# Optimization experiments

Hardware: AMD Instinct MI355X
Metric: run time of the kernel (lower is better)

Reference implementation:

```python
import jax, jax.numpy as jnp
import numpy as np

D_MODEL = 1024
D_STATE = 16
D_CONV = 4
EXPAND = 2
D_INNER = D_MODEL * EXPAND          # 2048
DT_RANK = max(1, D_MODEL // 16)     # 64
BATCH, SEQ = 4, 2048


def setup_inputs() -> dict:
    key = jax.random.key(0)
    ks = jax.random.split(key, 8)
    s = lambda n: 1.0 / np.sqrt(n)
    x = jax.random.normal(ks[0], (BATCH, SEQ, D_MODEL), jnp.float32)
    in_proj_w = jax.random.normal(ks[1], (2 * D_INNER, D_MODEL), jnp.float32) * s(D_MODEL)
    conv_w = jax.random.normal(ks[2], (D_INNER, 1, D_CONV), jnp.float32) * s(D_CONV)
    conv_b = jax.random.normal(ks[3], (D_INNER,), jnp.float32) * 0.01
    x_proj_w = jax.random.normal(ks[4], (DT_RANK + 2 * D_STATE, D_INNER), jnp.float32) * s(D_INNER)
    dt_proj_w = jax.random.normal(ks[5], (D_INNER, DT_RANK), jnp.float32) * s(DT_RANK)
    dt_proj_b = jax.random.normal(ks[6], (D_INNER,), jnp.float32) * 0.01
    A_log = jnp.broadcast_to(jnp.log(jnp.arange(1, D_STATE + 1, dtype=jnp.float32))[None, :],
                             (D_INNER, D_STATE)).copy()
    D_param = jnp.ones((D_INNER,), jnp.float32)
    out_proj_w = jax.random.normal(ks[7], (D_MODEL, D_INNER), jnp.float32) * s(D_INNER)
    return {"x": x, "in_proj_w": in_proj_w, "conv_w": conv_w, "conv_b": conv_b,
            "x_proj_w": x_proj_w, "dt_proj_w": dt_proj_w, "dt_proj_b": dt_proj_b,
            "A_log": A_log, "D_param": D_param, "out_proj_w": out_proj_w}


def _ssm_forward(x, in_proj_w, conv_w, conv_b, x_proj_w, dt_proj_w, dt_proj_b,
                 A_log, D_param, out_proj_w):
    B, L, _ = x.shape
    # input projection -> (B, L, 2*D_INNER), split into x_ssm and gate z
    xz = jnp.einsum('bld,ed->ble', x, in_proj_w)
    x_ssm, z = xz[..., :D_INNER], xz[..., D_INNER:]
    # causal depthwise conv1d (torch pads both sides then slices [:L] == left pad only)
    xc = jnp.transpose(x_ssm, (0, 2, 1))  # (B, D_INNER, L)
    xc = jax.lax.conv_general_dilated(
        xc, conv_w, window_strides=(1,), padding=[(D_CONV - 1, 0)],
        dimension_numbers=('NCH', 'OIH', 'NCH'), feature_group_count=D_INNER)
    xc = xc + conv_b[None, :, None]
    x_ssm = jax.nn.silu(jnp.transpose(xc, (0, 2, 1)))  # (B, L, D_INNER)
    # input-dependent dt, B, C
    dbl = jnp.einsum('bld,ed->ble', x_ssm, x_proj_w)  # (B, L, DT_RANK+2N)
    dt_x = dbl[..., :DT_RANK]
    B_x = dbl[..., DT_RANK:DT_RANK + D_STATE]
    C_x = dbl[..., DT_RANK + D_STATE:]
    dt = jax.nn.softplus(jnp.einsum('blr,dr->bld', dt_x, dt_proj_w) + dt_proj_b)  # (B, L, D_INNER)
    A = -jnp.exp(A_log)  # (D_INNER, D_STATE)

    # selective scan over L with lax.scan; carry h: (B, D_INNER, D_STATE)
    def step(h, inp):
        dt_t, B_t, C_t, x_t = inp  # (B,D), (B,N), (B,N), (B,D)
        dA = jnp.exp(dt_t[:, :, None] * A[None, :, :])          # (B, D, N)
        dB = dt_t[:, :, None] * B_t[:, None, :]                 # (B, D, N)
        h = dA * h + dB * x_t[:, :, None]
        y_t = jnp.einsum('bdn,bn->bd', h, C_t)
        return h, y_t

    h0 = jnp.zeros((B, D_INNER, D_STATE), x.dtype)
    xs = (jnp.moveaxis(dt, 1, 0), jnp.moveaxis(B_x, 1, 0),
          jnp.moveaxis(C_x, 1, 0), jnp.moveaxis(x_ssm, 1, 0))
    _, ys = jax.lax.scan(step, h0, xs)          # ys: (L, B, D_INNER)
    y = jnp.moveaxis(ys, 0, 1) + D_param[None, None, :] * x_ssm
    y = y * jax.nn.silu(z)
    return jnp.einsum('ble,de->bld', y, out_proj_w)


def reference(x, in_proj_w, conv_w, conv_b, x_proj_w, dt_proj_w, dt_proj_b,
              A_log, D_param, out_proj_w):
    return _ssm_forward(x, in_proj_w, conv_w, conv_b, x_proj_w, dt_proj_w,
                        dt_proj_b, A_log, D_param, out_proj_w)
```

## Files before the change

kernel.cpp:

```cpp
#include <hip/hip_runtime.h>
#include <hip/hip_bf16.h>
#include <math.h>

#define D_MODEL 1024
#define D_STATE 16
#define D_CONV 4
#define D_INNER 2048
#define DT_RANK 64
#define BATCH 4
#define SEQ 2048
#define ML (BATCH * SEQ)
#define NCH 64
#define CL (SEQ / NCH)

typedef __attribute__((ext_vector_type(8))) short short8;
typedef __attribute__((ext_vector_type(8))) unsigned short u16x8;
typedef __attribute__((ext_vector_type(4))) float f32x4;

__device__ __forceinline__ float bf2f(unsigned short u) {
  union { unsigned int i; float f; } v;
  v.i = ((unsigned int)u) << 16;
  return v.f;
}
__device__ __forceinline__ unsigned short f2bf(float f) {
  union { float f; unsigned int i; } u;
  u.f = f;
  unsigned int r = u.i + 0x7fffu + ((u.i >> 16) & 1u);
  return (unsigned short)(r >> 16);
}
__device__ __forceinline__ unsigned int f2bf_pk(float a, float b) {
  union { __hip_bfloat162 h; unsigned int u; } cv;
  cv.h = __float22bfloat162_rn(make_float2(a, b));
  return cv.u;
}
template <bool BF>
__device__ __forceinline__ float ld1(const void* p, size_t i) {
  if constexpr (BF) return bf2f(((const unsigned short*)p)[i]);
  else return ((const float*)p)[i];
}
template <bool BF>
__device__ __forceinline__ void ld4(const void* p, size_t i, float o[4]) {
  if constexpr (BF) {
    ushort4 v = *(const ushort4*)((const unsigned short*)p + i);
    o[0] = bf2f(v.x); o[1] = bf2f(v.y); o[2] = bf2f(v.z); o[3] = bf2f(v.w);
  } else {
    float4 v = *(const float4*)((const float*)p + i);
    o[0] = v.x; o[1] = v.y; o[2] = v.z; o[3] = v.w;
  }
}

__device__ __forceinline__ void gl_lds16(const unsigned short* g,
                                         unsigned short* l) {
  __builtin_amdgcn_global_load_lds(
      (const __attribute__((address_space(1))) void*)g,
      (__attribute__((address_space(3))) void*)l, 16, 0, 0);
}

#define CVT_N0 (ML * 1024)
#define CVT_N1 (4096 * 1024)
#define CVT_N2 (1024 * 2048)
#define CVT_N3 (2048 * 64)
#define CVT_N4 (128 * 2048)
#define CVT_E0 CVT_N0
#define CVT_E1 (CVT_E0 + CVT_N1)
#define CVT_E2 (CVT_E1 + CVT_N2)
#define CVT_E3 (CVT_E2 + CVT_N3)
#define CVT_E4 (CVT_E3 + CVT_N4)

__device__ __forceinline__ void cvt4(const void* in, size_t i,
                                     unsigned short* out, size_t o, int bf) {
  if (bf) {
    *(ushort4*)(out + o) = *(const ushort4*)((const unsigned short*)in + i);
  } else {
    float4 f = *(const float4*)((const float*)in + i);
    uint2 v;
    v.x = f2bf_pk(f.x, f.y);
    v.y = f2bf_pk(f.z, f.w);
    *(uint2*)(out + o) = v;
  }
}

__global__ __launch_bounds__(256) void cvt_all_kernel(
    const void* __restrict__ x, const void* __restrict__ ipw,
    const void* __restrict__ opw, const void* __restrict__ dtw,
    const void* __restrict__ xpw, unsigned short* __restrict__ x_bf,
    unsigned short* __restrict__ ipw_bf, unsigned short* __restrict__ opw_bf,
    unsigned short* __restrict__ dtw_bf, unsigned short* __restrict__ xpw_pad,
    int* __restrict__ flag) {
  __shared__ int cnt;
  if (threadIdx.x == 0) cnt = 0;
  __syncthreads();
  {
    const unsigned int wv = ((const unsigned int*)x)[threadIdx.x];
    const unsigned int e = (wv >> 7) & 0xffu;
    if (e < 100u || e > 145u) atomicAdd(&cnt, 1);
  }
  __syncthreads();
  const int bf = (cnt < 32) ? 1 : 0;
  if (blockIdx.x == 0 && threadIdx.x == 0) flag[0] = bf;

  const size_t g = (size_t)(blockIdx.x * 256 + threadIdx.x) * 4;
  if (g < CVT_E0) {
    cvt4(x, g, x_bf, g, bf);
  } else if (g < CVT_E1) {
    const size_t i = g - CVT_E0;
    cvt4(ipw, i, ipw_bf, i, bf);
  } else if (g < CVT_E2) {
    const size_t i = g - CVT_E1;
    cvt4(opw, i, opw_bf, i, bf);
  } else if (g < CVT_E3) {
    const size_t i = g - CVT_E2;
    cvt4(dtw, i, dtw_bf, i, bf);
  } else if (g < CVT_E4) {
    const size_t i = g - CVT_E3;
    const int row = (int)(i >> 11);
    if (row < 96) {
      cvt4(xpw, i, xpw_pad, i, bf);
    } else {
      ushort4 z = {0, 0, 0, 0};
      *(ushort4*)(xpw_pad + i) = z;
    }
  }
}

#define K1_LDA 1024
#define K1_NT 16

#define K1_STG(srcbase, lds, t_, h_)                                       \
  {                                                                        \
    const unsigned short* s_ =                                             \
        (srcbase) + (size_t)(h_) * (128 * K1_LDA) + (size_t)(t_) * 64;     \
    unsigned short* d_ = (lds) + (((t_) & 1) * 2 + (h_)) * 8192 + w * 512; \
    gl_lds16(s_, d_);                                                      \
    gl_lds16(s_ + 64 * K1_LDA, d_ + 4096);                                 \
  }

__global__ __launch_bounds__(512, 2) void gemm256_k1(
    const unsigned short* __restrict__ A,
    const unsigned short* __restrict__ B,
    unsigned short* __restrict__ C) {
  __shared__ unsigned short As[32768];
  __shared__ unsigned short Bs[32768];
  const int tid = threadIdx.x;
  const int l = tid & 63, w = tid >> 6;
  const int bid = blockIdx.x;
  const int swz = (bid & 7) * 64 + (bid >> 3);
  const int m0 = (swz >> 4) * 256, n0 = (swz & 15) * 256;
  const int row0 = tid >> 3;
  const int c0 = (tid & 7) ^ (row0 & 7);
  const unsigned short* aSrc = A + (size_t)(m0 + row0) * K1_LDA + c0 * 8;
  const unsigned short* bSrc = B + (size_t)(n0 + row0) * K1_LDA + c0 * 8;
  const int q = l >> 4, mr = l & 15;
  const int wm = w >> 2, wn = w & 3;

  K1_STG(aSrc, As, 0, 0);
  K1_STG(aSrc, As, 0, 1);
  K1_STG(bSrc, Bs, 0, 0);
  K1_STG(bSrc, Bs, 0, 1);
  K1_STG(bSrc, Bs, 1, 0);
  K1_STG(bSrc, Bs, 1, 1);
  K1_STG(aSrc, As, 1, 0);
  asm volatile("s_waitcnt vmcnt(6)" ::: "memory");
  asm volatile("s_barrier" ::: "memory");

  f32x4 acc[8][4] = {};
  for (int t = 0; t < K1_NT; ++t) {
    const int tb = (t & 1) * 2;
    short8 bfr[4][2];
#pragma unroll
    for (int ni = 0; ni < 4; ++ni)
#pragma unroll
      for (int kk = 0; kk < 2; ++kk) {
        const int r = (wn & 1) * 64 + ni * 16 + mr;
        const int c = kk * 4 + q;
        bfr[ni][kk] = *(const short8*)&Bs[(tb + (wn >> 1)) * 8192 + r * 64 +
                                          ((c ^ (r & 7)) * 8)];
      }
#pragma unroll
    for (int p = 0; p < 4; ++p) {
      short8 af[2][2];
#pragma unroll
      for (int i = 0; i < 2; ++i)
#pragma unroll
        for (int kk = 0; kk < 2; ++kk) {
          const int r = (2 * p + i) * 16 + mr;
          const int c = kk * 4 + q;
          af[i][kk] = *(const short8*)&As[(tb + wm) * 8192 + r * 64 +
                                          ((c ^ (r & 7)) * 8)];
        }
      if (p == 0) {
        if (t + 1 < K1_NT) K1_STG(aSrc, As, t + 1, 1);
      } else if (p == 1) {
        if (t + 2 < K1_NT) K1_STG(bSrc, Bs, t + 2, 0);
      } else if (p == 2) {
        if (t + 2 < K1_NT) K1_STG(bSrc, Bs, t + 2, 1);
      } else {
        if (t + 2 < K1_NT) K1_STG(aSrc, As, t + 2, 0);
      }
      asm volatile("s_barrier" ::: "memory");
      __builtin_amdgcn_s_setprio(1);
#pragma unroll
      for (int i = 0; i < 2; ++i)
#pragma unroll
        for (int ni = 0; ni < 4; ++ni)
#pragma unroll
          for (int kk = 0; kk < 2; ++kk)
            acc[2 * p + i][ni] = __builtin_amdgcn_mfma_f32_16x16x32_bf16(
                af[i][kk], bfr[ni][kk], acc[2 * p + i][ni], 0, 0, 0);
      __builtin_amdgcn_s_setprio(0);
      if (p == 3) {
        if (t + 2 < K1_NT) {
          asm volatile("s_waitcnt vmcnt(6)" ::: "memory");
        } else {
          asm volatile("s_waitcnt vmcnt(0)" ::: "memory");
        }
      }
      asm volatile("s_barrier" ::: "memory");
    }
  }
#pragma unroll
  for (int mi = 0; mi < 8; ++mi) {
#pragma unroll
    for (int ni = 0; ni < 4; ++ni) {
      const int row = m0 + wm * 128 + mi * 16 + q * 4;
      const int col = n0 + wn * 64 + ni * 16 + mr;
      const size_t off0 = (size_t)row * 4096 + col;
      const unsigned int p01 = f2bf_pk(acc[mi][ni][0], acc[mi][ni][1]);
      const unsigned int p23 = f2bf_pk(acc[mi][ni][2], acc[mi][ni][3]);
      C[off0] = (unsigned short)p01;
      C[off0 + 4096] = (unsigned short)(p01 >> 16);
      C[off0 + 2 * 4096] = (unsigned short)p23;
      C[off0 + 3 * 4096] = (unsigned short)(p23 >> 16);
    }
  }
}

#define K6_LDA 2048
#define K6_NT 32

#define K6_STGA(t_, h_)                                                 \
  {                                                                     \
    const unsigned short* s_ =                                          \
        aSrc + (size_t)(h_) * (128 * K6_LDA) + (size_t)(t_) * 64;       \
    unsigned short* d_ = As + (((t_) & 1) * 2 + (h_)) * 8192 + w * 512; \
    gl_lds16(s_, d_);                                                   \
    gl_lds16(s_ + 64 * K6_LDA, d_ + 4096);                              \
  }
#define K6_STGB(t_)                                            \
  {                                                            \
    const unsigned short* s_ = bSrc + (size_t)(t_) * 64;       \
    unsigned short* d_ = Bs6 + ((t_) & 1) * 8192 + w * 512;    \
    gl_lds16(s_, d_);                                          \
    gl_lds16(s_ + 64 * K6_LDA, d_ + 4096);                     \
  }

__global__ __launch_bounds__(512, 2) void gemm256x128_k6(
    const unsigned short* __restrict__ A,
    const unsigned short* __restrict__ B,
    void* __restrict__ C,
    const int* __restrict__ flag) {
  __shared__ unsigned short As[32768];
  __shared__ unsigned short Bs6[16384];
  const int tid = threadIdx.x;
  const int l = tid & 63, w = tid >> 6;
  const int bid = blockIdx.x;
  const int swz = (bid & 7) * 32 + (bid >> 3);
  const int n0 = (swz & 7) * 128, m0 = (swz >> 3) * 256;
  const int row0 = tid >> 3;
  const int c0 = (tid & 7) ^ (row0 & 7);
  const unsigned short* aSrc = A + (size_t)(m0 + row0) * K6_LDA + c0 * 8;
  const unsigned short* bSrc = B + (size_t)(n0 + row0) * K6_LDA + c0 * 8;
  const int q = l >> 4, mr = l & 15;
  const int wm = w >> 2, wn = w & 3;

  K6_STGA(0, 0);
  K6_STGA(0, 1);
  K6_STGB(0);
  K6_STGB(1);
  K6_STGA(1, 0);
  asm volatile("s_waitcnt vmcnt(4)" ::: "memory");
  asm volatile("s_barrier" ::: "memory");

  f32x4 acc[8][2] = {};
  for (int t = 0; t < K6_NT; ++t) {
    const int tb = (t & 1) * 2;
    short8 bfr[2][2];
#pragma unroll
    for (int ni = 0; ni < 2; ++ni)
#pragma unroll
      for (int kk = 0; kk < 2; ++kk) {
        const int r = wn * 32 + ni * 16 + mr;
        const int c = kk * 4 + q;
        bfr[ni][kk] = *(const short8*)&Bs6[(t & 1) * 8192 + r * 64 +
                                           ((c ^ (r & 7)) * 8)];
      }
#pragma unroll
    for (int p = 0; p < 4; ++p) {
      short8 af[2][2];
#pragma unroll
      for (int i = 0; i < 2; ++i)
#pragma unroll
        for (int kk = 0; kk < 2; ++kk) {
          const int r = (2 * p + i) * 16 + mr;
          const int c = kk * 4 + q;
          af[i][kk] = *(const short8*)&As[(tb + wm) * 8192 + r * 64 +
                                          ((c ^ (r & 7)) * 8)];
        }
      if (p == 0) {
        if (t + 1 < K6_NT) K6_STGA(t + 1, 1);
      } else if (p == 1) {
        if (t + 2 < K6_NT) K6_STGB(t + 2);
      } else if (p == 3) {
        if (t + 2 < K6_NT) K6_STGA(t + 2, 0);
      }
      asm volatile("s_barrier" ::: "memory");
      __builtin_amdgcn_s_setprio(1);
#pragma unroll
      for (int i = 0; i < 2; ++i)
#pragma unroll
        for (int ni = 0; ni < 2; ++ni)
#pragma unroll
          for (int kk = 0; kk < 2; ++kk)
            acc[2 * p + i][ni] = __builtin_amdgcn_mfma_f32_16x16x32_bf16(
                af[i][kk], bfr[ni][kk], acc[2 * p + i][ni], 0, 0, 0);
      __builtin_amdgcn_s_setprio(0);
      if (p == 3) {
        if (t + 2 < K6_NT) {
          asm volatile("s_waitcnt vmcnt(4)" ::: "memory");
        } else {
          asm volatile("s_waitcnt vmcnt(0)" ::: "memory");
        }
      }
      asm volatile("s_barrier" ::: "memory");
    }
  }
  const int bf = *flag;
#pragma unroll
  for (int mi = 0; mi < 8; ++mi) {
#pragma unroll
    for (int ni = 0; ni < 2; ++ni) {
      const int row = m0 + wm * 128 + mi * 16 + q * 4;
      const int col = n0 + wn * 32 + ni * 16 + mr;
      const size_t off0 = (size_t)row * 1024 + col;
      if (bf) {
        const unsigned int p01 = f2bf_pk(acc[mi][ni][0], acc[mi][ni][1]);
        const unsigned int p23 = f2bf_pk(acc[mi][ni][2], acc[mi][ni][3]);
        unsigned short* C16 = (unsigned short*)C;
        C16[off0] = (unsigned short)p01;
        C16[off0 + 1024] = (unsigned short)(p01 >> 16);
        C16[off0 + 2 * 1024] = (unsigned short)p23;
        C16[off0 + 3 * 1024] = (unsigned short)(p23 >> 16);
      } else {
        float* Cf = (float*)C;
#pragma unroll
        for (int j = 0; j < 4; ++j)
          Cf[off0 + (size_t)j * 1024] = acc[mi][ni][j];
      }
    }
  }
}

__global__ __launch_bounds__(256) void dt_gemm_kernel(
    const unsigned short* __restrict__ Adbl,
    const unsigned short* __restrict__ Bw,
    unsigned short* __restrict__ Cdt,
    const void* __restrict__ bias, const int* __restrict__ flag) {
  __shared__ unsigned short Bs[128 * 64];
  __shared__ unsigned short Ass[4][128 * 64];
  const int tid = threadIdx.x;
  const int l = tid & 63, w = tid >> 6;
  const int bn = blockIdx.x * 128;
  const int mg = blockIdx.y * 512;
  const int srow = tid >> 3;
  const int sc = ((tid & 7) ^ (srow & 7)) * 8;
  const unsigned short* aSrc = Adbl + (size_t)(mg + srow) * 128 + sc;
  const unsigned short* bSrc = Bw + (size_t)(bn + srow) * 64 + sc;
#define K4_STGB(i_) gl_lds16(bSrc + (i_) * 32 * 64, Bs + (i_)*2048 + w * 512)
#define K4_STGA(mt_, i_)                                  \
  gl_lds16(aSrc + (size_t)((mt_)*128 + (i_)*32) * 128,    \
           Ass[(mt_) & 3] + (i_)*2048 + w * 512)
  K4_STGB(0); K4_STGB(1); K4_STGB(2); K4_STGB(3);
  K4_STGA(0, 0); K4_STGA(0, 1); K4_STGA(0, 2); K4_STGA(0, 3);
  K4_STGA(1, 0); K4_STGA(1, 1); K4_STGA(1, 2); K4_STGA(1, 3);
  asm volatile("s_waitcnt vmcnt(4)" ::: "memory");
  asm volatile("s_barrier" ::: "memory");
  const int q = l >> 4, mr = l & 15;
  const int wm = w >> 1, wn = w & 1;
  short8 bfr[4][2];
#pragma unroll
  for (int ni = 0; ni < 4; ++ni)
#pragma unroll
    for (int kk = 0; kk < 2; ++kk) {
      const int r = wn * 64 + ni * 16 + mr;
      const int c = kk * 4 + q;
      bfr[ni][kk] = *(const short8*)&Bs[r * 64 + ((c ^ (r & 7)) * 8)];
    }
  const int bf = *flag;
  float bv[4];
#pragma unroll
  for (int ni = 0; ni < 4; ++ni) {
    const int col = bn + wn * 64 + ni * 16 + mr;
    bv[ni] = bf ? ld1<true>(bias, col) : ld1<false>(bias, col);
  }
#pragma unroll
  for (int mt = 0; mt < 4; ++mt) {
    if (mt + 2 < 4) {
      K4_STGA(mt + 2, 0); K4_STGA(mt + 2, 1);
      K4_STGA(mt + 2, 2); K4_STGA(mt + 2, 3);
    }
    short8 af[4][2];
#pragma unroll
    for (int mi = 0; mi < 4; ++mi)
#pragma unroll
      for (int kk = 0; kk < 2; ++kk) {
        const int r = wm * 64 + mi * 16 + mr;
        const int c = kk * 4 + q;
        af[mi][kk] =
            *(const short8*)&Ass[mt & 3][r * 64 + ((c ^ (r & 7)) * 8)];
      }
    f32x4 acc[4][4] = {};
#pragma unroll
    for (int mi = 0; mi < 4; ++mi)
#pragma unroll
      for (int ni = 0; ni < 4; ++ni)
#pragma unroll
        for (int kk = 0; kk < 2; ++kk)
          acc[mi][ni] = __builtin_amdgcn_mfma_f32_16x16x32_bf16(
              af[mi][kk], bfr[ni][kk], acc[mi][ni], 0, 0, 0);
#pragma unroll
    for (int mi = 0; mi < 4; ++mi) {
#pragma unroll
      for (int ni = 0; ni < 4; ++ni) {
        const int row = mg + mt * 128 + wm * 64 + mi * 16 + q * 4;
        const int col = bn + wn * 64 + ni * 16 + mr;
        const size_t off0 = (size_t)row * 4096 + col;
        float v[4];
#pragma unroll
        for (int j = 0; j < 4; ++j) {
          const float t = acc[mi][ni][j] + bv[ni];
          v[j] = fmaxf(t, 0.f) + __logf(1.f + __expf(-fabsf(t)));
        }
        const unsigned int p01 = f2bf_pk(v[0], v[1]);
        const unsigned int p23 = f2bf_pk(v[2], v[3]);
        Cdt[off0] = (unsigned short)p01;
        Cdt[off0 + 4096] = (unsigned short)(p01 >> 16);
        Cdt[off0 + 2 * 4096] = (unsigned short)p23;
        Cdt[off0 + 3 * 4096] = (unsigned short)(p23 >> 16);
      }
    }
    if (mt + 2 < 4) {
      asm volatile("s_waitcnt vmcnt(4)" ::: "memory");
    } else {
      asm volatile("s_waitcnt vmcnt(0)" ::: "memory");
    }
    if (mt < 3) asm volatile("s_barrier" ::: "memory");
  }
}

template <int EPI, int TAG>
__global__ __launch_bounds__(256) void gemm_mfma(
    const unsigned short* __restrict__ Ain, int lda,
    const unsigned short* __restrict__ Bin, int ldb, void* __restrict__ C,
    int ldc, int K, const void* __restrict__ bias,
    const int* __restrict__ flag) {
  __shared__ unsigned short As[128 * 32];
  __shared__ unsigned short Bs[128 * 32];
  const unsigned short* A = Ain;
  const unsigned short* B = Bin;
  if (EPI == 3) {
    A += (size_t)blockIdx.z * 512;
    B += (size_t)blockIdx.z * 512;
  }
  const int tid = threadIdx.x;
  const int l = tid & 63, w = tid >> 6;
  const int bm = blockIdx.y * 128;
  const int bn = blockIdx.x * 128;
  const int r0 = w * 16 + (l >> 2);
  const int cc = (((l & 3) ^ ((l >> 2) & 3) ^ ((l >> 4) & 3))) * 8;
  const unsigned short* Ap0 = A + (size_t)(bm + r0) * lda + cc;
  const unsigned short* Ap1 = A + (size_t)(bm + r0 + 64) * lda + cc;
  const unsigned short* Bp0 = B + (size_t)(bn + r0) * ldb + cc;
  const unsigned short* Bp1 = B + (size_t)(bn + r0 + 64) * ldb + cc;
  const int q = l >> 4, mr = l & 15;
  const int wm = w >> 1, wn = w & 1;
  const int slot = (q ^ (mr & 3) ^ (mr >> 2)) * 8;
  f32x4 acc[4][4] = {};
  for (int k0 = 0; k0 < K; k0 += 32) {
    gl_lds16(Ap0 + k0, As + w * 512);
    gl_lds16(Ap1 + k0, As + 2048 + w * 512);
    gl_lds16(Bp0 + k0, Bs + w * 512);
    gl_lds16(Bp1 + k0, Bs + 2048 + w * 512);
    __syncthreads();
    short8 af[4], bfr[4];
#pragma unroll
    for (int mi = 0; mi < 4; ++mi)
      af[mi] = *(const short8*)&As[(wm * 64 + mi * 16 + mr) * 32 + slot];
#pragma unroll
    for (int ni = 0; ni < 4; ++ni)
      bfr[ni] = *(const short8*)&Bs[(wn * 64 + ni * 16 + mr) * 32 + slot];
#pragma unroll
    for (int mi = 0; mi < 4; ++mi)
#pragma unroll
      for (int ni = 0; ni < 4; ++ni)
        acc[mi][ni] = __builtin_amdgcn_mfma_f32_16x16x32_bf16(
            af[mi], bfr[ni], acc[mi][ni], 0, 0, 0);
    __syncthreads();
  }
  const int bf = (EPI == 1) ? *flag : 0;
  float* Cp3 = (EPI == 3)
                   ? ((float*)C + (size_t)blockIdx.z * ML * 128)
                   : (float*)C;
#pragma unroll
  for (int mi = 0; mi < 4; ++mi) {
#pragma unroll
    for (int ni = 0; ni < 4; ++ni) {
      const int row = bm + wm * 64 + mi * 16 + q * 4;
      const int col = bn + wn * 64 + ni * 16 + mr;
      const size_t off0 = (size_t)row * ldc + col;
      if (EPI == 0) {
        const unsigned int p01 = f2bf_pk(acc[mi][ni][0], acc[mi][ni][1]);
        const unsigned int p23 = f2bf_pk(acc[mi][ni][2], acc[mi][ni][3]);
        unsigned short* C16 = (unsigned short*)C;
        C16[off0] = (unsigned short)p01;
        C16[off0 + ldc] = (unsigned short)(p01 >> 16);
        C16[off0 + 2 * (size_t)ldc] = (unsigned short)p23;
        C16[off0 + 3 * (size_t)ldc] = (unsigned short)(p23 >> 16);
      } else if (EPI == 3) {
#pragma unroll
        for (int j = 0; j < 4; ++j)
          Cp3[off0 + (size_t)j * ldc] = acc[mi][ni][j];
      } else {
        if (bf) {
          const unsigned int p01 = f2bf_pk(acc[mi][ni][0], acc[mi][ni][1]);
          const unsigned int p23 = f2bf_pk(acc[mi][ni][2], acc[mi][ni][3]);
          unsigned short* C16 = (unsigned short*)C;
          C16[off0] = (unsigned short)p01;
          C16[off0 + ldc] = (unsigned short)(p01 >> 16);
          C16[off0 + 2 * (size_t)ldc] = (unsigned short)p23;
          C16[off0 + 3 * (size_t)ldc] = (unsigned short)(p23 >> 16);
        } else {
          float* Cf = (float*)C;
#pragma unroll
          for (int j = 0; j < 4; ++j)
            Cf[off0 + (size_t)j * ldc] = acc[mi][ni][j];
        }
      }
    }
  }
}

__global__ __launch_bounds__(256) void reduceK3_kernel(
    const float* __restrict__ part, unsigned short* __restrict__ dbl) {
  const size_t i = (size_t)(blockIdx.x * 256 + threadIdx.x) * 4;
  const size_t st = (size_t)ML * 128;
  float4 a = *(const float4*)(part + i);
  float4 b = *(const float4*)(part + st + i);
  float4 c = *(const float4*)(part + 2 * st + i);
  float4 d = *(const float4*)(part + 3 * st + i);
  uint2 v;
  v.x = f2bf_pk(a.x + b.x + c.x + d.x, a.y + b.y + c.y + d.y);
  v.y = f2bf_pk(a.z + b.z + c.z + d.z, a.w + b.w + c.w + d.w);
  *(uint2*)(dbl + i) = v;
}

__global__ __launch_bounds__(256) void conv_silu_kernel(
    const unsigned short* __restrict__ xzb, const void* __restrict__ cw,
    const void* __restrict__ cb, unsigned short* __restrict__ xcb,
    const int* __restrict__ flag) {
  const int bf = *flag;
  const int e = (blockIdx.x * 256 + threadIdx.x) * 4;
  const int d = e & (D_INNER - 1);
  const int bl = e >> 11;
  const int l = bl & (SEQ - 1);
  const size_t base = (size_t)bl * 4096 + d;
  float x0[4], x1[4] = {}, x2[4] = {}, x3[4] = {};
  ld4<true>(xzb, base, x0);
  if (l >= 1) ld4<true>(xzb, base - 4096, x1);
  if (l >= 2) ld4<true>(xzb, base - 2 * 4096, x2);
  if (l >= 3) ld4<true>(xzb, base - 3 * 4096, x3);
  float r[4];
#pragma unroll
  for (int i = 0; i < 4; ++i) {
    float w[4];
    if (bf) ld4<true>(cw, (size_t)(d + i) * 4, w);
    else ld4<false>(cw, (size_t)(d + i) * 4, w);
    const float bias = bf ? ld1<true>(cb, d + i) : ld1<false>(cb, d + i);
    float acc = bias + w[3] * x0[i] + w[2] * x1[i] + w[1] * x2[i] + w[0] * x3[i];
    r[i] = acc / (1.f + __expf(-acc));
  }
  uint2 o;
  o.x = f2bf_pk(r[0], r[1]);
  o.y = f2bf_pk(r[2], r[3]);
  *(uint2*)(xcb + e) = o;
}

__device__ __forceinline__ void load_a(const void* A_log, int bf, int d,
                                       float a[16], float& dev) {
  float t[4];
#pragma unroll
  for (int k = 0; k < 4; ++k) {
    if (bf) ld4<true>(A_log, (size_t)d * 16 + k * 4, t);
    else ld4<false>(A_log, (size_t)d * 16 + k * 4, t);
#pragma unroll
    for (int j = 0; j < 4; ++j) a[k * 4 + j] = -expf(t[j]);
  }
  dev = 0.f;
#pragma unroll
  for (int n = 0; n < 16; ++n) dev = fmaxf(dev, fabsf(a[n] + (float)(n + 1)));
}

__device__ __forceinline__ void pow_tree(float e1, float pw[16]) {
  const float e2 = e1 * e1;
  const float e3 = e2 * e1;
  const float e4 = e2 * e2;
  pw[0] = e1; pw[1] = e2; pw[2] = e3; pw[3] = e4;
  pw[4] = e4 * e1; pw[5] = e4 * e2; pw[6] = e4 * e3; pw[7] = e4 * e4;
  const float e8 = pw[7];
  pw[8] = e8 * e1; pw[9] = e8 * e2; pw[10] = e8 * e3; pw[11] = e8 * e4;
  pw[12] = e8 * pw[4]; pw[13] = e8 * pw[5]; pw[14] = e8 * pw[6];
  pw[15] = e8 * e8;
}

__global__ __launch_bounds__(256) void scan_passA(
    const unsigned short* __restrict__ xzb,
    const unsigned short* __restrict__ xcb,
    const unsigned short* __restrict__ dbl, const void* __restrict__ A_log,
    const int* __restrict__ flag, float* __restrict__ S,
    float* __restrict__ Sdt) {
  const int bf = *flag;
  const int gid = blockIdx.x * 256 + threadIdx.x;
  const int d = gid & (D_INNER - 1);
  const int c = (gid >> 11) & (NCH - 1);
  const int b = gid >> 17;
  float a[16], dev;
  load_a(A_log, bf, d, a, dev);
  float h[16] = {};
  float sdt = 0.f;
  const size_t m0 = (size_t)b * SEQ + c * CL;
  if (dev < 1e-3f) {
    for (int t = 0; t < CL; ++t) {
      const size_t m = m0 + t;
      const float dtv = bf2f(xzb[m * 4096 + d]);
      const float xv = bf2f(xcb[m * 2048 + d]);
      const u16x8 B0 = *(const u16x8*)&dbl[m * 128 + 64];
      const u16x8 B1 = *(const u16x8*)&dbl[m * 128 + 72];
      const float dtx = dtv * xv;
      sdt += dtv;
      float pw[16];
      pow_tree(__expf(-dtv), pw);
#pragma unroll
      for (int n = 0; n < 16; ++n) {
        const float Bv = bf2f(n < 8 ? B0[n] : B1[n - 8]);
        h[n] = fmaf(pw[n], h[n], Bv * dtx);
      }
    }
  } else {
    for (int t = 0; t < CL; ++t) {
      const size_t m = m0 + t;
      const float dtv = bf2f(xzb[m * 4096 + d]);
      const float xv = bf2f(xcb[m * 2048 + d]);
      const u16x8 B0 = *(const u16x8*)&dbl[m * 128 + 64];
      const u16x8 B1 = *(const u16x8*)&dbl[m * 128 + 72];
      const float dtx = dtv * xv;
      sdt += dtv;
#pragma unroll
      for (int n = 0; n < 16; ++n) {
        const float Bv = bf2f(n < 8 ? B0[n] : B1[n - 8]);
        h[n] = fmaf(__expf(dtv * a[n]), h[n], Bv * dtx);
      }
    }
  }
  const size_t sbase = (((size_t)b * NCH + c) * 16) * D_INNER + d;
#pragma unroll
  for (int n = 0; n < 16; ++n) S[sbase + (size_t)n * D_INNER] = h[n];
  Sdt[((size_t)b * NCH + c) * D_INNER + d] = sdt;
}

__global__ __launch_bounds__(256) void scan_passB(
    float* __restrict__ S, const float* __restrict__ Sdt,
    const void* __restrict__ A_log, const int* __restrict__ flag) {
  const int bf = *flag;
  const int idx = blockIdx.x * 256 + threadIdx.x;
  const int d = idx & (D_INNER - 1);
  const int n = (idx >> 11) & 15;
  const int b = idx >> 15;
  const float al = bf ? ld1<true>(A_log, (size_t)d * 16 + n)
                      : ld1<false>(A_log, (size_t)d * 16 + n);
  const float a = -expf(al);
  float h = 0.f;
  for (int c = 0; c < NCH; ++c) {
    const size_t base = ((size_t)b * NCH + c);
    const size_t sidx = (base * 16 + n) * D_INNER + d;
    const float s = S[sidx];
    const float sdt = Sdt[base * D_INNER + d];
    const float p = __expf(a * sdt);
    S[sidx] = h;
    h = p * h + s;
  }
}

__global__ __launch_bounds__(256) void scan_passC(
    const unsigned short* __restrict__ xzb,
    const unsigned short* __restrict__ xcb,
    const unsigned short* __restrict__ dbl, const void* __restrict__ A_log,
    const void* __restrict__ Dp, const float* __restrict__ S,
    const int* __restrict__ flag, unsigned short* __restrict__ ybf) {
  const int bf = *flag;
  const int gid = blockIdx.x * 256 + threadIdx.x;
  const int d = gid & (D_INNER - 1);
  const int c = (gid >> 11) & (NCH - 1);
  const int b = gid >> 17;
  float a[16], dev;
  load_a(A_log, bf, d, a, dev);
  const float Dv = bf ? ld1<true>(Dp, d) : ld1<false>(Dp, d);
  float h[16];
  const size_t sbase = (((size_t)b * NCH + c) * 16) * D_INNER + d;
#pragma unroll
  for (int n = 0; n < 16; ++n) h[n] = S[sbase + (size_t)n * D_INNER];
  const size_t m0 = (size_t)b * SEQ + c * CL;
  const bool trick = dev < 1e-3f;
  for (int t = 0; t < CL; ++t) {
    const size_t m = m0 + t;
    const float dtv = bf2f(xzb[m * 4096 + d]);
    const float xv = bf2f(xcb[m * 2048 + d]);
    const u16x8 B0 = *(const u16x8*)&dbl[m * 128 + 64];
    const u16x8 B1 = *(const u16x8*)&dbl[m * 128 + 72];
    const u16x8 C0 = *(const u16x8*)&dbl[m * 128 + 80];
    const u16x8 C1 = *(const u16x8*)&dbl[m * 128 + 88];
    const float dtx = dtv * xv;
    float y = 0.f;
    if (trick) {
      float pw[16];
      pow_tree(__expf(-dtv), pw);
#pragma unroll
      for (int n = 0; n < 16; ++n) {
        const float Bv = bf2f(n < 8 ? B0[n] : B1[n - 8]);
        const float Cv = bf2f(n < 8 ? C0[n] : C1[n - 8]);
        h[n] = fmaf(pw[n], h[n], Bv * dtx);
        y = fmaf(h[n], Cv, y);
      }
    } else {
#pragma unroll
      for (int n = 0; n < 16; ++n) {
        const float Bv = bf2f(n < 8 ? B0[n] : B1[n - 8]);
        const float Cv = bf2f(n < 8 ? C0[n] : C1[n - 8]);
        h[n] = fmaf(__expf(dtv * a[n]), h[n], Bv * dtx);
        y = fmaf(h[n], Cv, y);
      }
    }
    const float zv = bf2f(xzb[m * 4096 + 2048 + d]);
    const float yv = y + Dv * xv;
    ybf[m * 2048 + d] = f2bf(yv * (zv / (1.f + __expf(-zv))));
  }
}

extern "C" void kernel_launch(void* const* d_in, const int* in_sizes, int n_in,
                              void* d_out, int out_size, void* d_ws,
                              size_t ws_size, hipStream_t stream) {
  const void* x = d_in[0];
  const void* in_proj_w = d_in[1];
  const void* conv_w = d_in[2];
  const void* conv_b = d_in[3];
  const void* x_proj_w = d_in[4];
  const void* dt_proj_w = d_in[5];
  const void* dt_proj_b = d_in[6];
  const void* A_log = d_in[7];
  const void* D_param = d_in[8];
  const void* out_proj_w = d_in[9];

  char* wsb = (char*)d_ws;
  int* flag = (int*)wsb;
  unsigned short* xzb = (unsigned short*)(wsb + 256);
  unsigned short* xcb = xzb + (size_t)ML * 4096;
  unsigned short* dbl = xcb + (size_t)ML * 2048;
  unsigned short* ybf = dbl + (size_t)ML * 128;
  float* S = (float*)(ybf + (size_t)ML * 2048);
  float* Sdt = S + (size_t)BATCH * NCH * D_INNER * 16;
  unsigned short* opw_bf =
      (unsigned short*)(Sdt + (size_t)BATCH * NCH * D_INNER * 16);
  unsigned short* xpw_pad = opw_bf + (size_t)1024 * 2048;
  unsigned short* dtw_bf = xpw_pad + (size_t)128 * 2048;
  unsigned short* x_bf = xcb;
  unsigned short* ipw_bf = xcb + (size_t)ML * 1024;
  float* k3part = S;

  cvt_all_kernel<<<CVT_E4 / 1024, 256, 0, stream>>>(
      x, in_proj_w, out_proj_w, dt_proj_w, x_proj_w, x_bf, ipw_bf, opw_bf,
      dtw_bf, xpw_pad, flag);
  gemm256_k1<<<dim3(512), 512, 0, stream>>>(x_bf, ipw_bf, xzb);
  conv_silu_kernel<<<(ML * D_INNER) / 1024, 256, 0, stream>>>(
      xzb, conv_w, conv_b, xcb, flag);
  {
    dim3 g(1, ML / 128, 4);
    gemm_mfma<3, 3><<<g, 256, 0, stream>>>(xcb, 2048, xpw_pad, 2048, k3part,
                                           128, 512, nullptr, flag);
  }
  reduceK3_kernel<<<(ML * 128) / 1024, 256, 0, stream>>>(k3part, dbl);
  dt_gemm_kernel<<<dim3(16, 16), 256, 0, stream>>>(dbl, dtw_bf, xzb,
                                                   dt_proj_b, flag);
  scan_passA<<<(BATCH * NCH * D_INNER) / 256, 256, 0, stream>>>(
      xzb, xcb, dbl, A_log, flag, S, Sdt);
  scan_passB<<<(BATCH * D_INNER * 16) / 256, 256, 0, stream>>>(S, Sdt, A_log,
                                                               flag);
  scan_passC<<<(BATCH * NCH * D_INNER) / 256, 256, 0, stream>>>(
      xzb, xcb, dbl, A_log, D_param, S, flag, ybf);
  gemm256x128_k6<<<dim3(256), 512, 0, stream>>>(ybf, opw_bf, d_out, flag);
}
```

Before: 438.1 us.

## Replace split-K x_proj GEMM and reduction with a pipelined single-pass kernel; halve scan chunks

The x_proj GEMM used to be split four ways along K, with each split writing fp32 partial sums and a separate reduce kernel summing them. A new xproj_gemm kernel instead computes each 32x128 output tile over the full K. It uses a 4-stage LDS ring with asynchronous global-to-LDS loads and writes bf16 straight into dbl. This removes the fp32 partial-sum round trip through memory and one kernel launch, at the cost of only 256 blocks doing longer serial K loops. The scan chunk count also drops from 64 to 32, which halves the parallelism in scan passes A and C while shortening the sequential carry pass B, and the workspace layout is shrunk to match.

Result: no change. 445.7 us (+1.7%).

```diff
diff --git a/kernel.cpp b/kernel.cpp
--- a/kernel.cpp
+++ b/kernel.cpp
@@ -10,7 +10,8 @@
 #define BATCH 4
 #define SEQ 2048
 #define ML (BATCH * SEQ)
-#define NCH 64
+#define NCH 32
+#define LOG_NCH 5
 #define CL (SEQ / NCH)
 
 typedef __attribute__((ext_vector_type(8))) short short8;
@@ -357,6 +358,87 @@
           Cf[off0 + (size_t)j * 1024] = acc[mi][ni][j];
       }
     }
+  }
+}
+
+#define K3_NT 32
+
+#define K3_STGA(t_)                                                        \
+  gl_lds16(aSrc + (size_t)(t_) * 64, As3 + ((t_) & 3) * 2048 + w * 512)
+#define K3_STGB(t_, i_)                                                    \
+  gl_lds16(bSrc + (size_t)(i_) * 32 * 2048 + (size_t)(t_) * 64,            \
+           Bs3 + ((t_) & 3) * 8192 + (i_) * 2048 + w * 512)
+#define K3_STG_ALL(t_)                                                     \
+  { K3_STGA(t_); K3_STGB(t_, 0); K3_STGB(t_, 1); K3_STGB(t_, 2);           \
+    K3_STGB(t_, 3); }
+
+__global__ __launch_bounds__(256) void xproj_gemm(
+    const unsigned short* __restrict__ A,
+    const unsigned short* __restrict__ B,
+    unsigned short* __restrict__ C) {
+  __shared__ unsigned short As3[4 * 32 * 64];
+  __shared__ unsigned short Bs3[4 * 128 * 64];
+  const int tid = threadIdx.x;
+  const int l = tid & 63, w = tid >> 6;
+  const int bid = blockIdx.x;
+  const int swz = (bid & 7) * 32 + (bid >> 3);
+  const int m0 = swz * 32;
+  const int row0 = tid >> 3;
+  const int c0 = (tid & 7) ^ (row0 & 7);
+  const unsigned short* aSrc = A + (size_t)(m0 + row0) * 2048 + c0 * 8;
+  const unsigned short* bSrc = B + (size_t)row0 * 2048 + c0 * 8;
+  const int q = l >> 4, mr = l & 15;
+  const int wm = w >> 1, wn = w & 1;
+
+  K3_STG_ALL(0);
+  K3_STG_ALL(1);
+  asm volatile("s_waitcnt vmcnt(5)" ::: "memory");
+  asm volatile("s_barrier" ::: "memory");
+
+  f32x4 acc[4] = {};
+  for (int t = 0; t < K3_NT; ++t) {
+    if (t + 2 < K3_NT) K3_STG_ALL(t + 2);
+    short8 af[2], bfr[4][2];
+#pragma unroll
+    for (int kk = 0; kk < 2; ++kk) {
+      const int r = wm * 16 + mr;
+      const int c = kk * 4 + q;
+      af[kk] = *(const short8*)&As3[(t & 3) * 2048 + r * 64 +
+                                    ((c ^ (r & 7)) * 8)];
+    }
+#pragma unroll
+    for (int ni = 0; ni < 4; ++ni)
+#pragma unroll
+      for (int kk = 0; kk < 2; ++kk) {
+        const int r = wn * 64 + ni * 16 + mr;
+        const int c = kk * 4 + q;
+        bfr[ni][kk] = *(const short8*)&Bs3[(t & 3) * 8192 + r * 64 +
+                                           ((c ^ (r & 7)) * 8)];
+      }
+#pragma unroll
+    for (int ni = 0; ni < 4; ++ni)
+#pragma unroll
+      for (int kk = 0; kk < 2; ++kk)
+        acc[ni] = __builtin_amdgcn_mfma_f32_16x16x32_bf16(af[kk], bfr[ni][kk],
+                                                          acc[ni], 0, 0, 0);
+    if (t + 2 < K3_NT) {
+      asm volatile("s_waitcnt vmcnt(5)" ::: "memory");
+    } else {
+      asm volatile("s_waitcnt vmcnt(0)" ::: "memory");
+    }
+    asm volatile("s_barrier" ::: "memory");
+  }
+#pragma unroll
+  for (int ni = 0; ni < 4; ++ni) {
+    const int row = m0 + wm * 16 + q * 4;
+    const int col = wn * 64 + ni * 16 + mr;
+    const size_t off0 = (size_t)row * 128 + col;
+    const unsigned int p01 = f2bf_pk(acc[ni][0], acc[ni][1]);
+    const unsigned int p23 = f2bf_pk(acc[ni][2], acc[ni][3]);
+    C[off0] = (unsigned short)p01;
+    C[off0 + 128] = (unsigned short)(p01 >> 16);
+    C[off0 + 2 * 128] = (unsigned short)p23;
+    C[off0 + 3 * 128] = (unsigned short)(p23 >> 16);
   }
 }
 
@@ -457,112 +539,6 @@
   }
 }
 
-template <int EPI, int TAG>
-__global__ __launch_bounds__(256) void gemm_mfma(
-    const unsigned short* __restrict__ Ain, int lda,
-    const unsigned short* __restrict__ Bin, int ldb, void* __restrict__ C,
-    int ldc, int K, const void* __restrict__ bias,
-    const int* __restrict__ flag) {
-  __shared__ unsigned short As[128 * 32];
-  __shared__ unsigned short Bs[128 * 32];
-  const unsigned short* A = Ain;
-  const unsigned short* B = Bin;
-  if (EPI == 3) {
-    A += (size_t)blockIdx.z * 512;
-    B += (size_t)blockIdx.z * 512;
-  }
-  const int tid = threadIdx.x;
-  const int l = tid & 63, w = tid >> 6;
-  const int bm = blockIdx.y * 128;
-  const int bn = blockIdx.x * 128;
-  const int r0 = w * 16 + (l >> 2);
-  const int cc = (((l & 3) ^ ((l >> 2) & 3) ^ ((l >> 4) & 3))) * 8;
-  const unsigned short* Ap0 = A + (size_t)(bm + r0) * lda + cc;
-  const unsigned short* Ap1 = A + (size_t)(bm + r0 + 64) * lda + cc;
-  const unsigned short* Bp0 = B + (size_t)(bn + r0) * ldb + cc;
-  const unsigned short* Bp1 = B + (size_t)(bn + r0 + 64) * ldb + cc;
-  const int q = l >> 4, mr = l & 15;
-  const int wm = w >> 1, wn = w & 1;
-  const int slot = (q ^ (mr & 3) ^ (mr >> 2)) * 8;
-  f32x4 acc[4][4] = {};
-  for (int k0 = 0; k0 < K; k0 += 32) {
-    gl_lds16(Ap0 + k0, As + w * 512);
-    gl_lds16(Ap1 + k0, As + 2048 + w * 512);
-    gl_lds16(Bp0 + k0, Bs + w * 512);
-    gl_lds16(Bp1 + k0, Bs + 2048 + w * 512);
-    __syncthreads();
-    short8 af[4], bfr[4];
-#pragma unroll
-    for (int mi = 0; mi < 4; ++mi)
-      af[mi] = *(const short8*)&As[(wm * 64 + mi * 16 + mr) * 32 + slot];
-#pragma unroll
-    for (int ni = 0; ni < 4; ++ni)
-      bfr[ni] = *(const short8*)&Bs[(wn * 64 + ni * 16 + mr) * 32 + slot];
-#pragma unroll
-    for (int mi = 0; mi < 4; ++mi)
-#pragma unroll
-      for (int ni = 0; ni < 4; ++ni)
-        acc[mi][ni] = __builtin_amdgcn_mfma_f32_16x16x32_bf16(
-            af[mi], bfr[ni], acc[mi][ni], 0, 0, 0);
-    __syncthreads();
-  }
-  const int bf = (EPI == 1) ? *flag : 0;
-  float* Cp3 = (EPI == 3)
-                   ? ((float*)C + (size_t)blockIdx.z * ML * 128)
-                   : (float*)C;
-#pragma unroll
-  for (int mi = 0; mi < 4; ++mi) {
-#pragma unroll
-    for (int ni = 0; ni < 4; ++ni) {
-      const int row = bm + wm * 64 + mi * 16 + q * 4;
-      const int col = bn + wn * 64 + ni * 16 + mr;
-      const size_t off0 = (size_t)row * ldc + col;
-      if (EPI == 0) {
-        const unsigned int p01 = f2bf_pk(acc[mi][ni][0], acc[mi][ni][1]);
-        const unsigned int p23 = f2bf_pk(acc[mi][ni][2], acc[mi][ni][3]);
-        unsigned short* C16 = (unsigned short*)C;
-        C16[off0] = (unsigned short)p01;
-        C16[off0 + ldc] = (unsigned short)(p01 >> 16);
-        C16[off0 + 2 * (size_t)ldc] = (unsigned short)p23;
-        C16[off0 + 3 * (size_t)ldc] = (unsigned short)(p23 >> 16);
-      } else if (EPI == 3) {
-#pragma unroll
-        for (int j = 0; j < 4; ++j)
-          Cp3[off0 + (size_t)j * ldc] = acc[mi][ni][j];
-      } else {
-        if (bf) {
-          const unsigned int p01 = f2bf_pk(acc[mi][ni][0], acc[mi][ni][1]);
-          const unsigned int p23 = f2bf_pk(acc[mi][ni][2], acc[mi][ni][3]);
-          unsigned short* C16 = (unsigned short*)C;
-          C16[off0] = (unsigned short)p01;
-          C16[off0 + ldc] = (unsigned short)(p01 >> 16);
-          C16[off0 + 2 * (size_t)ldc] = (unsigned short)p23;
-          C16[off0 + 3 * (size_t)ldc] = (unsigned short)(p23 >> 16);
-        } else {
-          float* Cf = (float*)C;
-#pragma unroll
-          for (int j = 0; j < 4; ++j)
-            Cf[off0 + (size_t)j * ldc] = acc[mi][ni][j];
-        }
-      }
-    }
-  }
-}
-
-__global__ __launch_bounds__(256) void reduceK3_kernel(
-    const float* __restrict__ part, unsigned short* __restrict__ dbl) {
-  const size_t i = (size_t)(blockIdx.x * 256 + threadIdx.x) * 4;
-  const size_t st = (size_t)ML * 128;
-  float4 a = *(const float4*)(part + i);
-  float4 b = *(const float4*)(part + st + i);
-  float4 c = *(const float4*)(part + 2 * st + i);
-  float4 d = *(const float4*)(part + 3 * st + i);
-  uint2 v;
-  v.x = f2bf_pk(a.x + b.x + c.x + d.x, a.y + b.y + c.y + d.y);
-  v.y = f2bf_pk(a.z + b.z + c.z + d.z, a.w + b.w + c.w + d.w);
-  *(uint2*)(dbl + i) = v;
-}
-
 __global__ __launch_bounds__(256) void conv_silu_kernel(
     const unsigned short* __restrict__ xzb, const void* __restrict__ cw,
     const void* __restrict__ cb, unsigned short* __restrict__ xcb,
@@ -631,7 +607,7 @@
   const int gid = blockIdx.x * 256 + threadIdx.x;
   const int d = gid & (D_INNER - 1);
   const int c = (gid >> 11) & (NCH - 1);
-  const int b = gid >> 17;
+  const int b = gid >> (11 + LOG_NCH);
   float a[16], dev;
   load_a(A_log, bf, d, a, dev);
   float h[16] = {};
@@ -709,7 +685,7 @@
   const int gid = blockIdx.x * 256 + threadIdx.x;
   const int d = gid & (D_INNER - 1);
   const int c = (gid >> 11) & (NCH - 1);
-  const int b = gid >> 17;
+  const int b = gid >> (11 + LOG_NCH);
   float a[16], dev;
   load_a(A_log, bf, d, a, dev);
   const float Dv = bf ? ld1<true>(Dp, d) : ld1<false>(Dp, d);
@@ -777,12 +753,11 @@
   float* S = (float*)(ybf + (size_t)ML * 2048);
   float* Sdt = S + (size_t)BATCH * NCH * D_INNER * 16;
   unsigned short* opw_bf =
-      (unsigned short*)(Sdt + (size_t)BATCH * NCH * D_INNER * 16);
+      (unsigned short*)(Sdt + (size_t)BATCH * NCH * D_INNER);
   unsigned short* xpw_pad = opw_bf + (size_t)1024 * 2048;
   unsigned short* dtw_bf = xpw_pad + (size_t)128 * 2048;
   unsigned short* x_bf = xcb;
   unsigned short* ipw_bf = xcb + (size_t)ML * 1024;
-  float* k3part = S;
 
   cvt_all_kernel<<<CVT_E4 / 1024, 256, 0, stream>>>(
       x, in_proj_w, out_proj_w, dt_proj_w, x_proj_w, x_bf, ipw_bf, opw_bf,
@@ -790,12 +765,7 @@
   gemm256_k1<<<dim3(512), 512, 0, stream>>>(x_bf, ipw_bf, xzb);
   conv_silu_kernel<<<(ML * D_INNER) / 1024, 256, 0, stream>>>(
       xzb, conv_w, conv_b, xcb, flag);
-  {
-    dim3 g(1, ML / 128, 4);
-    gemm_mfma<3, 3><<<g, 256, 0, stream>>>(xcb, 2048, xpw_pad, 2048, k3part,
-                                           128, 512, nullptr, flag);
-  }
-  reduceK3_kernel<<<(ML * 128) / 1024, 256, 0, stream>>>(k3part, dbl);
+  xproj_gemm<<<dim3(256), 256, 0, stream>>>(xcb, xpw_pad, dbl);
   dt_gemm_kernel<<<dim3(16, 16), 256, 0, stream>>>(dbl, dtw_bf, xzb,
                                                    dt_proj_b, flag);
   scan_passA<<<(BATCH * NCH * D_INNER) / 256, 256, 0, stream>>>(
```
